# Kernel tuning notes

Hardware: AMD Instinct MI355X
Metric: run time of the kernel (lower is better)

## Reference

```python
import jax, jax.numpy as jnp
import numpy as np

N, M, D, K = 50000, 32, 128, 8
DELTA_D = D // K
EPS = 1e-12  # torch F.normalize eps


def _normalize(v, axis):
    nrm = jnp.linalg.norm(v, axis=axis, keepdims=True)
    return v / jnp.maximum(nrm, EPS)


def setup_inputs() -> dict:
    key = jax.random.key(0)
    k1, k2 = jax.random.split(key)
    x = jax.random.normal(k1, (N, D), dtype=jnp.float32)
    neighbors = jax.random.randint(k2, (N * M,), 0, N + 1, dtype=jnp.int64)
    return {"x": x, "neighbors": neighbors, "max_iter": 6}


def reference(x, neighbors, max_iter):
    n, d = x.shape
    m = neighbors.shape[0] // n
    k, delta_d = K, DELTA_D
    # per-capsule L2 normalize input features
    x = _normalize(x.reshape(n, k, delta_d), axis=2).reshape(n, d)
    # append zero row for padding index n, gather neighbor features
    z = jnp.concatenate([x, jnp.zeros((1, d), dtype=x.dtype)], axis=0)
    z = z[neighbors].reshape(n, m, k, delta_d)
    x_c = x.reshape(n, k, delta_d)
    u = None
    for it in range(max_iter):
        if u is None:
            p = jnp.zeros((n, m, k), dtype=x.dtype)
        else:
            p = jnp.einsum('nmkd,nkd->nmk', z, u)
        p = jax.nn.softmax(p, axis=2)
        u = jnp.einsum('nmkd,nmk->nkd', z, p) + x_c
        if it < max_iter - 1:
            u = _normalize(u, axis=2)
    return u.reshape(n, d)
```

## Files before the change

kernel.cpp:

```cpp
#include <hip/hip_runtime.h>
#include <math.h>


constexpr int NROWS = 50000;
constexpr int MN = 32;
constexpr int DDIM = 128;
constexpr float FEPS = 1e-12f;

template <int CTRL>
__device__ __forceinline__ float dpp_mov(float v) {
    int r = __builtin_amdgcn_update_dpp(0, __builtin_bit_cast(int, v), CTRL, 0xF, 0xF, true);
    return __builtin_bit_cast(float, r);
}

__device__ __forceinline__ float inv_norm(float ss) {
    float r = rsqrtf(fmaxf(ss, FEPS * FEPS));
    return r;
}

__device__ __forceinline__ void normalize16(float (&u)[16]) {
    float s0 = 0.f, s1 = 0.f;
#pragma unroll
    for (int d = 0; d < 16; d += 2) {
        s0 = fmaf(u[d], u[d], s0);
        s1 = fmaf(u[d + 1], u[d + 1], s1);
    }
    float iv = inv_norm(s0 + s1);
#pragma unroll
    for (int d = 0; d < 16; ++d) u[d] *= iv;
}

__device__ __forceinline__ void reduce_bcast_j(float (&u)[16]) {
#pragma unroll
    for (int d = 0; d < 16; ++d) u[d] += dpp_mov<0xB1>(u[d]);
#pragma unroll
    for (int d = 0; d < 16; ++d) u[d] += dpp_mov<0x4E>(u[d]);
#pragma unroll
    for (int d = 0; d < 16; ++d) u[d] += __shfl_xor(u[d], 4);
}

__global__ __launch_bounds__(256, 4) void routing_kernel(const float* __restrict__ x,
                                                         const int* __restrict__ nbr,
                                                         float* __restrict__ out) {
    const int lane = threadIdx.x & 63;
    const int n = blockIdx.x * 4 + (threadIdx.x >> 6);
    const int j = lane & 7;
    const int k = lane >> 3;

    float xc[16];
    {
        const float4* p = reinterpret_cast<const float4*>(x + (size_t)n * DDIM + k * 16);
#pragma unroll
        for (int q = 0; q < 4; ++q) {
            float4 v = p[q];
            xc[4 * q + 0] = v.x; xc[4 * q + 1] = v.y;
            xc[4 * q + 2] = v.z; xc[4 * q + 3] = v.w;
        }
        normalize16(xc);
    }

    float z[4][16];
    {
        const int* __restrict__ nrow = nbr + (size_t)n * MN;
        int idx[4];
#pragma unroll
        for (int t = 0; t < 4; ++t) idx[t] = nrow[j + 8 * t];
#pragma unroll
        for (int t = 0; t < 4; ++t) {
            if (idx[t] < NROWS) {
                const float4* p =
                    reinterpret_cast<const float4*>(x + (size_t)idx[t] * DDIM + k * 16);
#pragma unroll
                for (int q = 0; q < 4; ++q) {
                    float4 v = p[q];
                    z[t][4 * q + 0] = v.x; z[t][4 * q + 1] = v.y;
                    z[t][4 * q + 2] = v.z; z[t][4 * q + 3] = v.w;
                }
            } else {
#pragma unroll
                for (int d = 0; d < 16; ++d) z[t][d] = 0.f;
            }
            normalize16(z[t]);
        }
    }

    float u[16];
#pragma unroll
    for (int d = 0; d < 16; ++d)
        u[d] = 0.125f * ((z[0][d] + z[1][d]) + (z[2][d] + z[3][d]));
    reduce_bcast_j(u);
#pragma unroll
    for (int d = 0; d < 16; ++d) u[d] += xc[d];
    normalize16(u);

#pragma unroll
    for (int it = 1; it < 6; ++it) {
        float pn[4];
#pragma unroll
        for (int t = 0; t < 4; ++t) {
            float a = 0.f, b = 0.f;
#pragma unroll
            for (int d = 0; d < 16; d += 2) {
                a = fmaf(z[t][d], u[d], a);
                b = fmaf(z[t][d + 1], u[d + 1], b);
            }
            float p = a + b;
            float e = __expf(p);
            float s = e + dpp_mov<0x128>(e);
            s += __shfl_xor(s, 16);
            s += __shfl_xor(s, 32);
            pn[t] = e * __frcp_rn(s);
        }
#pragma unroll
        for (int d = 0; d < 16; ++d) {
            float a = z[0][d] * pn[0];
            a = fmaf(z[1][d], pn[1], a);
            a = fmaf(z[2][d], pn[2], a);
            a = fmaf(z[3][d], pn[3], a);
            u[d] = a;
        }
        reduce_bcast_j(u);
#pragma unroll
        for (int d = 0; d < 16; ++d) u[d] += xc[d];
        if (it < 5) normalize16(u);
    }

    if (j < 4) {
        float4 w;
        w.x = (j == 0) ? u[0] : (j == 1) ? u[4] : (j == 2) ? u[8]  : u[12];
        w.y = (j == 0) ? u[1] : (j == 1) ? u[5] : (j == 2) ? u[9]  : u[13];
        w.z = (j == 0) ? u[2] : (j == 1) ? u[6] : (j == 2) ? u[10] : u[14];
        w.w = (j == 0) ? u[3] : (j == 1) ? u[7] : (j == 2) ? u[11] : u[15];
        *reinterpret_cast<float4*>(out + (size_t)n * DDIM + k * 16 + 4 * j) = w;
    }
}

extern "C" void kernel_launch(void* const* d_in, const int* in_sizes, int n_in,
                              void* d_out, int out_size, void* d_ws, size_t ws_size,
                              hipStream_t stream) {
    const float* x = (const float*)d_in[0];
    const int* nbr = (const int*)d_in[1];
    float* out = (float*)d_out;
    routing_kernel<<<NROWS / 4, 256, 0, stream>>>(x, nbr, out);
}
```

Measured before the change: 224.5 us.

## Prenormalize features in a separate pass and fold normalization into softmax scale

Adds a prepass kernel that normalizes every row (plus a zero padding row) into workspace, so the routing kernel gathers already-normalized neighbours without branches or per-neighbour normalization. Instead of normalizing u each iteration, it keeps u unnormalized and folds the inverse norm and log2e into an exp2 scale. It also folds xc into the FMA chain, swaps in hardware rcp/rsq/exp2 builtins, and has all 64 lanes write the output as float2. The cost is an extra launch and a full read and write of x, and the approximate intrinsics may change precision slightly.

```diff
diff --git a/kernel.cpp b/kernel.cpp
--- a/kernel.cpp
+++ b/kernel.cpp
@@ -5,41 +5,93 @@
 constexpr int NROWS = 50000;
 constexpr int MN = 32;
 constexpr int DDIM = 128;
-constexpr float FEPS = 1e-12f;
+constexpr float FEPS2 = 1e-24f;
+constexpr float LOG2E = 1.44269504088896340736f;
+
+#if __has_builtin(__builtin_amdgcn_rcpf)
+__device__ __forceinline__ float fast_rcp(float v) { return __builtin_amdgcn_rcpf(v); }
+#else
+__device__ __forceinline__ float fast_rcp(float v) { return __frcp_rn(v); }
+#endif
+#if __has_builtin(__builtin_amdgcn_rsqf)
+__device__ __forceinline__ float fast_rsq(float v) { return __builtin_amdgcn_rsqf(v); }
+#else
+__device__ __forceinline__ float fast_rsq(float v) { return rsqrtf(v); }
+#endif
+#if __has_builtin(__builtin_amdgcn_exp2f)
+__device__ __forceinline__ float fast_exp2(float v) { return __builtin_amdgcn_exp2f(v); }
+#else
+__device__ __forceinline__ float fast_exp2(float v) { return exp2f(v); }
+#endif
 
 template <int CTRL>
-__device__ __forceinline__ float dpp_mov(float v) {
+__device__ __forceinline__ float dpp_add(float v) {
     int r = __builtin_amdgcn_update_dpp(0, __builtin_bit_cast(int, v), CTRL, 0xF, 0xF, true);
-    return __builtin_bit_cast(float, r);
+    return v + __builtin_bit_cast(float, r);
 }
 
-__device__ __forceinline__ float inv_norm(float ss) {
-    float r = rsqrtf(fmaxf(ss, FEPS * FEPS));
-    return r;
+__device__ __forceinline__ void load16(float (&dst)[16], const float* __restrict__ p) {
+    const float4* q = reinterpret_cast<const float4*>(p);
+#pragma unroll
+    for (int i = 0; i < 4; ++i) {
+        float4 v = q[i];
+        dst[4 * i + 0] = v.x; dst[4 * i + 1] = v.y;
+        dst[4 * i + 2] = v.z; dst[4 * i + 3] = v.w;
+    }
 }
 
-__device__ __forceinline__ void normalize16(float (&u)[16]) {
-    float s0 = 0.f, s1 = 0.f;
+__device__ __forceinline__ void normalize16(float (&v)[16]) {
+    float a = v[0] * v[0], b = v[1] * v[1];
 #pragma unroll
-    for (int d = 0; d < 16; d += 2) {
-        s0 = fmaf(u[d], u[d], s0);
-        s1 = fmaf(u[d + 1], u[d + 1], s1);
+    for (int d = 2; d < 16; d += 2) {
+        a = fmaf(v[d], v[d], a);
+        b = fmaf(v[d + 1], v[d + 1], b);
     }
-    float iv = inv_norm(s0 + s1);
+    float iv = fast_rsq(fmaxf(a + b, FEPS2));
 #pragma unroll
-    for (int d = 0; d < 16; ++d) u[d] *= iv;
+    for (int d = 0; d < 16; ++d) v[d] *= iv;
 }
 
-__device__ __forceinline__ void reduce_bcast_j(float (&u)[16]) {
+__device__ __forceinline__ void butterfly8(float (&u)[16]) {
 #pragma unroll
-    for (int d = 0; d < 16; ++d) u[d] += dpp_mov<0xB1>(u[d]);
+    for (int d = 0; d < 16; ++d) u[d] = dpp_add<0xB1>(u[d]);
 #pragma unroll
-    for (int d = 0; d < 16; ++d) u[d] += dpp_mov<0x4E>(u[d]);
+    for (int d = 0; d < 16; ++d) u[d] = dpp_add<0x4E>(u[d]);
 #pragma unroll
     for (int d = 0; d < 16; ++d) u[d] += __shfl_xor(u[d], 4);
 }
 
-__global__ __launch_bounds__(256, 4) void routing_kernel(const float* __restrict__ x,
+__device__ __forceinline__ float inv_norm_log2e(const float (&u)[16]) {
+    float a = u[0] * u[0], b = u[1] * u[1];
+#pragma unroll
+    for (int d = 2; d < 16; d += 2) {
+        a = fmaf(u[d], u[d], a);
+        b = fmaf(u[d + 1], u[d + 1], b);
+    }
+    return fast_rsq(fmaxf(a + b, FEPS2)) * LOG2E;
+}
+
+__global__ __launch_bounds__(256) void norm_kernel(const float* __restrict__ x,
+                                                   float* __restrict__ xn) {
+    int t = blockIdx.x * 256 + threadIdx.x;
+    constexpr int TOTAL = (NROWS + 1) * (DDIM / 4);
+    if (t >= TOTAL) return;
+    int n = t >> 5;
+    float4 v = make_float4(0.f, 0.f, 0.f, 0.f);
+    if (n < NROWS) v = reinterpret_cast<const float4*>(x)[t];
+    float ss = v.x * v.x;
+    ss = fmaf(v.y, v.y, ss);
+    ss = fmaf(v.z, v.z, ss);
+    ss = fmaf(v.w, v.w, ss);
+    ss = dpp_add<0xB1>(ss);
+    ss = dpp_add<0x4E>(ss);
+    float iv = fast_rsq(fmaxf(ss, FEPS2));
+    v.x *= iv; v.y *= iv; v.z *= iv; v.w *= iv;
+    reinterpret_cast<float4*>(xn)[t] = v;
+}
+
+template <bool PRENORM>
+__global__ __launch_bounds__(256, 4) void routing_kernel(const float* __restrict__ xsrc,
                                                          const int* __restrict__ nbr,
                                                          float* __restrict__ out) {
     const int lane = threadIdx.x & 63;
@@ -47,92 +99,81 @@
     const int j = lane & 7;
     const int k = lane >> 3;
 
-    float xc[16];
-    {
-        const float4* p = reinterpret_cast<const float4*>(x + (size_t)n * DDIM + k * 16);
+    float xc8[16];
+    load16(xc8, xsrc + n * DDIM + k * 16);
+    if (!PRENORM) normalize16(xc8);
 #pragma unroll
-        for (int q = 0; q < 4; ++q) {
-            float4 v = p[q];
-            xc[4 * q + 0] = v.x; xc[4 * q + 1] = v.y;
-            xc[4 * q + 2] = v.z; xc[4 * q + 3] = v.w;
-        }
-        normalize16(xc);
-    }
+    for (int d = 0; d < 16; ++d) xc8[d] *= 0.125f;
 
     float z[4][16];
     {
-        const int* __restrict__ nrow = nbr + (size_t)n * MN;
+        const int* __restrict__ nrow = nbr + n * MN;
         int idx[4];
 #pragma unroll
         for (int t = 0; t < 4; ++t) idx[t] = nrow[j + 8 * t];
 #pragma unroll
         for (int t = 0; t < 4; ++t) {
-            if (idx[t] < NROWS) {
-                const float4* p =
-                    reinterpret_cast<const float4*>(x + (size_t)idx[t] * DDIM + k * 16);
+            if (PRENORM) {
+                load16(z[t], xsrc + idx[t] * DDIM + k * 16);
+            } else {
+                if (idx[t] < NROWS) {
+                    load16(z[t], xsrc + idx[t] * DDIM + k * 16);
+                    normalize16(z[t]);
+                } else {
 #pragma unroll
-                for (int q = 0; q < 4; ++q) {
-                    float4 v = p[q];
-                    z[t][4 * q + 0] = v.x; z[t][4 * q + 1] = v.y;
-                    z[t][4 * q + 2] = v.z; z[t][4 * q + 3] = v.w;
+                    for (int d = 0; d < 16; ++d) z[t][d] = 0.f;
                 }
-            } else {
-#pragma unroll
-                for (int d = 0; d < 16; ++d) z[t][d] = 0.f;
             }
-            normalize16(z[t]);
         }
     }
 
     float u[16];
 #pragma unroll
-    for (int d = 0; d < 16; ++d)
-        u[d] = 0.125f * ((z[0][d] + z[1][d]) + (z[2][d] + z[3][d]));
-    reduce_bcast_j(u);
-#pragma unroll
-    for (int d = 0; d < 16; ++d) u[d] += xc[d];
-    normalize16(u);
+    for (int d = 0; d < 16; ++d) {
+        float a = fmaf(z[0][d], 0.125f, xc8[d]);
+        a = fmaf(z[1][d], 0.125f, a);
+        a = fmaf(z[2][d], 0.125f, a);
+        a = fmaf(z[3][d], 0.125f, a);
+        u[d] = a;
+    }
+    butterfly8(u);
+    float c = inv_norm_log2e(u);
 
 #pragma unroll
     for (int it = 1; it < 6; ++it) {
         float pn[4];
 #pragma unroll
         for (int t = 0; t < 4; ++t) {
-            float a = 0.f, b = 0.f;
+            float a = z[t][0] * u[0], b = z[t][1] * u[1];
 #pragma unroll
-            for (int d = 0; d < 16; d += 2) {
+            for (int d = 2; d < 16; d += 2) {
                 a = fmaf(z[t][d], u[d], a);
                 b = fmaf(z[t][d + 1], u[d + 1], b);
             }
-            float p = a + b;
-            float e = __expf(p);
-            float s = e + dpp_mov<0x128>(e);
+            float e = fast_exp2((a + b) * c);
+            float s = dpp_add<0x128>(e);
             s += __shfl_xor(s, 16);
             s += __shfl_xor(s, 32);
-            pn[t] = e * __frcp_rn(s);
+            pn[t] = e * fast_rcp(s);
         }
 #pragma unroll
         for (int d = 0; d < 16; ++d) {
-            float a = z[0][d] * pn[0];
+            float a = fmaf(z[0][d], pn[0], xc8[d]);
             a = fmaf(z[1][d], pn[1], a);
             a = fmaf(z[2][d], pn[2], a);
             a = fmaf(z[3][d], pn[3], a);
             u[d] = a;
         }
-        reduce_bcast_j(u);
-#pragma unroll
-        for (int d = 0; d < 16; ++d) u[d] += xc[d];
-        if (it < 5) normalize16(u);
+        butterfly8(u);
+        if (it < 5) c = inv_norm_log2e(u);
     }
 
-    if (j < 4) {
-        float4 w;
-        w.x = (j == 0) ? u[0] : (j == 1) ? u[4] : (j == 2) ? u[8]  : u[12];
-        w.y = (j == 0) ? u[1] : (j == 1) ? u[5] : (j == 2) ? u[9]  : u[13];
-        w.z = (j == 0) ? u[2] : (j == 1) ? u[6] : (j == 2) ? u[10] : u[14];
-        w.w = (j == 0) ? u[3] : (j == 1) ? u[7] : (j == 2) ? u[11] : u[15];
-        *reinterpret_cast<float4*>(out + (size_t)n * DDIM + k * 16 + 4 * j) = w;
+    float w0 = u[0], w1 = u[1];
+#pragma unroll
+    for (int d = 1; d < 8; ++d) {
+        if (j == d) { w0 = u[2 * d]; w1 = u[2 * d + 1]; }
     }
+    *reinterpret_cast<float2*>(out + n * DDIM + 2 * lane) = make_float2(w0, w1);
 }
 
 extern "C" void kernel_launch(void* const* d_in, const int* in_sizes, int n_in,
@@ -141,5 +182,14 @@
     const float* x = (const float*)d_in[0];
     const int* nbr = (const int*)d_in[1];
     float* out = (float*)d_out;
-    routing_kernel<<<NROWS / 4, 256, 0, stream>>>(x, nbr, out);
+
+    const size_t need = (size_t)(NROWS + 1) * DDIM * sizeof(float);
+    if (ws_size >= need) {
+        float* xn = (float*)d_ws;
+        constexpr int TOTAL = (NROWS + 1) * (DDIM / 4);
+        norm_kernel<<<(TOTAL + 255) / 256, 256, 0, stream>>>(x, xn);
+        routing_kernel<true><<<NROWS / 4, 256, 0, stream>>>(xn, nbr, out);
+    } else {
+        routing_kernel<false><<<NROWS / 4, 256, 0, stream>>>(x, nbr, out);
+    }
 }
```

Result: faster. 203.4 us (-9.4%).
